# Performance work log

Hardware: AMD Instinct MI355X
Metric: run time of the kernel (lower is better)

## Reference

```python
import jax, jax.numpy as jnp
import numpy as np

N = 50000
E = 800000
EPS = 1e-5
GAT_SLOPE = 0.2   # PyG GATConv internal LeakyReLU slope
ACT_SLOPE = 0.01  # decoder's LeakyReLU(alpha)


def setup_inputs() -> dict:
    key = jax.random.key(0)
    ks = jax.random.split(key, 10)
    d = {
        "embeddings": jax.random.normal(ks[0], (N, 64), jnp.float32),
        "edge_index": jax.random.randint(ks[1], (2, E), 0, N, jnp.int64),
        "W1": jax.random.normal(ks[2], (64, 128), jnp.float32) * 0.1,
        "a_src1": jax.random.normal(ks[3], (128,), jnp.float32) * 0.1,
        "a_dst1": jax.random.normal(ks[4], (128,), jnp.float32) * 0.1,
        "b1": jnp.zeros((128,), jnp.float32),
        "gamma1": jnp.ones((128,), jnp.float32),
        "beta1": jnp.zeros((128,), jnp.float32),
        "W2": jax.random.normal(ks[5], (128, 256), jnp.float32) * 0.1,
        "a_src2": jax.random.normal(ks[6], (256,), jnp.float32) * 0.1,
        "a_dst2": jax.random.normal(ks[7], (256,), jnp.float32) * 0.1,
        "b2": jnp.zeros((256,), jnp.float32),
        "gamma2": jnp.ones((256,), jnp.float32),
        "beta2": jnp.zeros((256,), jnp.float32),
        "Wf": jax.random.normal(ks[8], (256, 256), jnp.float32) * 0.1,
        "bf": jnp.zeros((256,), jnp.float32),
    }
    return d


def gat_conv(x, src, dst, W, a_s, a_d, b):
    # PyG GATConv, heads=1, concat=False, add_self_loops=True (loops appended in caller)
    h = x @ W                                    # [N, out]
    e = h @ a_s                                  # alpha_src per node
    f = h @ a_d                                  # alpha_dst per node
    logits = jax.nn.leaky_relu(e[src] + f[dst], GAT_SLOPE)   # [E']
    # scatter-softmax over destination neighborhoods
    m = jax.ops.segment_max(logits, dst, num_segments=N)
    ex = jnp.exp(logits - m[dst])
    denom = jax.ops.segment_sum(ex, dst, num_segments=N)
    alpha = ex / denom[dst]                      # [E']
    out = jax.ops.segment_sum(h[src] * alpha[:, None], dst, num_segments=N)
    return out + b


def batch_norm(x, gamma, beta):
    mu = jnp.mean(x, axis=0)
    var = jnp.mean((x - mu) ** 2, axis=0)        # biased, as torch BN uses
    return (x - mu) * jax.lax.rsqrt(var + EPS) * gamma + beta


def reference(embeddings, edge_index, W1, a_src1, a_dst1, b1, gamma1, beta1,
              W2, a_src2, a_dst2, b2, gamma2, beta2, Wf, bf):
    loops = jnp.arange(N, dtype=edge_index.dtype)
    src = jnp.concatenate([edge_index[0], loops])
    dst = jnp.concatenate([edge_index[1], loops])
    x = embeddings
    for (W, a_s, a_d, b, g, be) in [
        (W1, a_src1, a_dst1, b1, gamma1, beta1),
        (W2, a_src2, a_dst2, b2, gamma2, beta2),
    ]:
        x = gat_conv(x, src, dst, W, a_s, a_d, b)
        x = batch_norm(x, g, be)
        x = jax.nn.leaky_relu(x, ACT_SLOPE)
        # dropout: identity (eval mode)
    return x @ Wf + bf
```

## Files before the change

kernel.cpp:

```cpp
#include <hip/hip_runtime.h>
#include <hip/hip_fp16.h>
#include <math.h>

#define N_NODES 50000
#define N_EDGES 800000
#define N_TOT   850000
#define EPS_BN  1e-5f
#define GAT_SLOPE 0.2f
#define ACT_SLOPE 0.01f
#define NBUCK   ((N_NODES + 255) / 256)
#define BCAP    5120
#define K1_CH   4096
#define K1_NB   ((N_TOT + K1_CH - 1) / K1_CH)
#define GB64    ((N_NODES + 63) / 64)

typedef _Float16 half8_t __attribute__((ext_vector_type(8)));
typedef _Float16 half4_t __attribute__((ext_vector_type(4)));
typedef _Float16 half2_t __attribute__((ext_vector_type(2)));
typedef float    f32x4   __attribute__((ext_vector_type(4)));

__device__ __forceinline__ float wred_max(float x) {
#pragma unroll
    for (int m = 32; m; m >>= 1) x = fmaxf(x, __shfl_xor(x, m, 64));
    return x;
}
__device__ __forceinline__ float wred_sum(float x) {
#pragma unroll
    for (int m = 32; m; m >>= 1) x += __shfl_xor(x, m, 64);
    return x;
}
__device__ __forceinline__ int wred_sum_i(int x) {
#pragma unroll
    for (int m = 32; m; m >>= 1) x += __shfl_xor(x, m, 64);
    return x;
}

__device__ __forceinline__ void wf_perm(const float* __restrict__ W,
                                        _Float16* __restrict__ wt,
                                        int K, int C, int i) {
    int j   = i & 7;
    int l   = (i >> 3) & 63;
    int rest = i >> 9;
    int tt  = rest & 3;
    int ksf = rest >> 2;
    int KS  = K >> 5;
    int cb  = ksf / KS, ks = ksf - cb * KS;
    int k   = ks * 32 + (l >> 4) * 8 + j;
    int c   = cb * 64 + tt * 16 + (l & 15);
    wt[i] = (_Float16)W[k * C + c];
}

__global__ void init_misc(const float* __restrict__ W1, const float* __restrict__ W2,
                          const float* __restrict__ Wf, _Float16* __restrict__ wt1,
                          _Float16* __restrict__ wt2, _Float16* __restrict__ wtf,
                          int* __restrict__ bcnt,
                          const float* __restrict__ as1, const float* __restrict__ ad1,
                          const float* __restrict__ as2, const float* __restrict__ ad2,
                          float* __restrict__ va1, float* __restrict__ vb1,
                          float* __restrict__ va2, float* __restrict__ vb2) {
    int i = blockIdx.x * 256 + threadIdx.x;
    if (i < NBUCK) bcnt[i] = 0;
    if (i < 8192) {
        wf_perm(W1, wt1, 64, 128, i);
    } else if (i < 8192 + 32768) {
        wf_perm(W2, wt2, 128, 256, i - 8192);
    } else if (i < 8192 + 32768 + 65536) {
        wf_perm(Wf, wtf, 256, 256, i - 40960);
    } else if (i < 106496 + 384) {
        int j = i - 106496;
        if (j < 64) {
            float s = 0.f;
            for (int c = 0; c < 128; ++c) s += W1[j * 128 + c] * as1[c];
            va1[j] = s;
        } else if (j < 128) {
            int k = j - 64; float s = 0.f;
            for (int c = 0; c < 128; ++c) s += W1[k * 128 + c] * ad1[c];
            vb1[k] = s;
        } else if (j < 256) {
            int k = j - 128; float s = 0.f;
            for (int c = 0; c < 256; ++c) s += W2[k * 256 + c] * as2[c];
            va2[k] = s;
        } else {
            int k = j - 256; float s = 0.f;
            for (int c = 0; c < 256; ++c) s += W2[k * 256 + c] * ad2[c];
            vb2[k] = s;
        }
    }
}

__global__ __launch_bounds__(256) void
emb_dots(const float* __restrict__ emb, const float* __restrict__ va,
         const float* __restrict__ vb, _Float16* __restrict__ embh,
         float* __restrict__ e_n, float* __restrict__ f_n) {
    int r = blockIdx.x * 4 + (threadIdx.x >> 6);
    if (r >= N_NODES) return;
    int l = threadIdx.x & 63;
    float v = emb[(size_t)r * 64 + l];
    embh[(size_t)r * 64 + l] = (_Float16)v;
    float pe = wred_sum(v * va[l]);
    float pf = wred_sum(v * vb[l]);
    if (l == 0) { e_n[r] = pe; f_n[r] = pf; }
}

__global__ __launch_bounds__(256) void
ef_dots(const _Float16* __restrict__ x, const float* __restrict__ sc,
        const float* __restrict__ sh, const float* __restrict__ va,
        const float* __restrict__ vb, _Float16* __restrict__ z,
        float* __restrict__ e_n, float* __restrict__ f_n) {
    int r = blockIdx.x * 4 + (threadIdx.x >> 6);
    if (r >= N_NODES) return;
    int l = threadIdx.x & 63;
    int c = 2 * l;
    half2_t hv = *(const half2_t*)&x[(size_t)r * 128 + c];
    float x0 = (float)hv[0] * sc[c] + sh[c];
    float x1 = (float)hv[1] * sc[c + 1] + sh[c + 1];
    x0 = x0 > 0.f ? x0 : ACT_SLOPE * x0;
    x1 = x1 > 0.f ? x1 : ACT_SLOPE * x1;
    half2_t zo = { (_Float16)x0, (_Float16)x1 };
    *(half2_t*)&z[(size_t)r * 128 + c] = zo;
    float pe = wred_sum(x0 * va[c] + x1 * va[c + 1]);
    float pf = wred_sum(x0 * vb[c] + x1 * vb[c + 1]);
    if (l == 0) { e_n[r] = pe; f_n[r] = pf; }
}

template<int K, int C, int CB, typename InT, typename OutT, bool STATS>
__global__ __launch_bounds__(256) void
gemm_mfma(const InT* __restrict__ x, const _Float16* __restrict__ wt,
          const float* __restrict__ bias, OutT* __restrict__ out, int n,
          const float* __restrict__ scale, const float* __restrict__ shift,
          float2* __restrict__ pbn) {
    constexpr int NW_C = CB / 64;
    constexpr int RT   = NW_C;
    constexpr int NCB  = C / CB;
    constexpr int KS   = K / 32;
    constexpr int LK   = K + 8;
    constexpr int LCB  = CB + 4;
    constexpr size_t SMB = ((size_t)64 * LK * 2 > (size_t)64 * LCB * 4)
                             ? (size_t)64 * LK * 2 : (size_t)64 * LCB * 4;
    __shared__ alignas(16) char smem[SMB];
    _Float16* xs  = (_Float16*)smem;
    float*   cbuf = (float*)smem;
    __shared__ float cs_sh[STATS ? CB : 1];
    __shared__ float cq_sh[STATS ? CB : 1];

    const int rb = blockIdx.x / NCB;
    const int cblk = blockIdx.x - rb * NCB;
    const int row0 = rb * 64;
    const int colB = cblk * CB;
    const int t = threadIdx.x;

    if (STATS) {
        for (int c = t; c < CB; c += 256) { cs_sh[c] = 0.f; cq_sh[c] = 0.f; }
    }

    if constexpr (__is_same(InT, _Float16)) {
        for (int i = t * 8; i < 64 * K; i += 256 * 8) {
            int r = i / K, c = i - (i / K) * K;
            half8_t v = {};
            if (row0 + r < n) v = *(const half8_t*)&x[(size_t)(row0 + r) * K + c];
            if (scale) {
#pragma unroll
                for (int j = 0; j < 8; ++j) {
                    float f = (float)v[j] * scale[c + j] + shift[c + j];
                    v[j] = (_Float16)(f > 0.f ? f : ACT_SLOPE * f);
                }
            }
            *(half8_t*)&xs[r * LK + c] = v;
        }
    } else {
        for (int i = t * 4; i < 64 * K; i += 256 * 4) {
            int r = i / K, c = i - (i / K) * K;
            float4 v = make_float4(0.f, 0.f, 0.f, 0.f);
            if (row0 + r < n) v = *(const float4*)&x[(size_t)(row0 + r) * K + c];
            if (scale) {
                v.x = v.x * scale[c] + shift[c];         v.x = v.x > 0.f ? v.x : ACT_SLOPE * v.x;
                v.y = v.y * scale[c + 1] + shift[c + 1]; v.y = v.y > 0.f ? v.y : ACT_SLOPE * v.y;
                v.z = v.z * scale[c + 2] + shift[c + 2]; v.z = v.z > 0.f ? v.z : ACT_SLOPE * v.z;
                v.w = v.w * scale[c + 3] + shift[c + 3]; v.w = v.w > 0.f ? v.w : ACT_SLOPE * v.w;
            }
            half4_t h4 = { (_Float16)v.x, (_Float16)v.y, (_Float16)v.z, (_Float16)v.w };
            *(half4_t*)&xs[r * LK + c] = h4;
        }
    }
    __syncthreads();

    const int w = t >> 6, l = t & 63;
    const int l16 = l & 15, quad = l >> 4;
    const int lc0 = (w % NW_C) * 64;
    const int gc0 = colB + lc0;
    const int mbase = (w / NW_C) * (16 * NW_C);
    const _Float16* wtw = wt + (size_t)(gc0 >> 6) * KS * 4 * 512 + l * 8;

    f32x4 acc[RT][4] = {};
    half8_t bA[4], bB[4];
    auto loadB = [&](int k0, half8_t* bf) {
        const _Float16* p = wtw + (size_t)(k0 >> 5) * 4 * 512;
#pragma unroll
        for (int tt = 0; tt < 4; ++tt)
            bf[tt] = *(const half8_t*)&p[tt * 512];
    };
    auto doMM = [&](int k0, half8_t* bf) {
        half8_t a[RT];
#pragma unroll
        for (int rt = 0; rt < RT; ++rt)
            a[rt] = *(const half8_t*)&xs[(mbase + rt * 16 + l16) * LK + k0 + quad * 8];
#pragma unroll
        for (int rt = 0; rt < RT; ++rt)
#pragma unroll
            for (int tt = 0; tt < 4; ++tt)
                acc[rt][tt] = __builtin_amdgcn_mfma_f32_16x16x32_f16(a[rt], bf[tt],
                                                                     acc[rt][tt], 0, 0, 0);
    };
    loadB(0, bA);
#pragma unroll
    for (int k0 = 0; k0 < K; k0 += 64) {
        loadB(k0 + 32, bB);
        doMM(k0, bA);
        if (k0 + 64 < K) loadB(k0 + 64, bA);
        doMM(k0 + 32, bB);
    }

    __syncthreads();
#pragma unroll
    for (int rt = 0; rt < RT; ++rt) {
#pragma unroll
        for (int tt = 0; tt < 4; ++tt) {
            int lcol = lc0 + tt * 16 + l16;
            float bb = bias ? bias[colB + lcol] : 0.f;
            float s = 0.f, q = 0.f;
#pragma unroll
            for (int i = 0; i < 4; ++i) {
                int lrow = mbase + rt * 16 + quad * 4 + i;
                float v = acc[rt][tt][i] + bb;
                cbuf[lrow * LCB + lcol] = v;
                if (STATS && row0 + lrow < n) { s += v; q += v * v; }
            }
            if constexpr (STATS) {
                s += __shfl_xor(s, 16, 64); s += __shfl_xor(s, 32, 64);
                q += __shfl_xor(q, 16, 64); q += __shfl_xor(q, 32, 64);
                if (quad == 0) {
                    atomicAdd(&cs_sh[lcol], s);
                    atomicAdd(&cq_sh[lcol], q);
                }
            }
        }
    }
    __syncthreads();
    if constexpr (STATS) {
        for (int c = t; c < CB; c += 256)
            pbn[(size_t)rb * C + colB + c] = make_float2(cs_sh[c], cq_sh[c]);
    }
    for (int i = t * 4; i < 64 * CB; i += 256 * 4) {
        int r = i / CB, c = i - (i / CB) * CB;
        if (row0 + r < n) {
            float4 v4 = *(const float4*)&cbuf[r * LCB + c];
            if constexpr (__is_same(OutT, float)) {
                *(float4*)&out[(size_t)(row0 + r) * C + colB + c] = v4;
            } else {
                half4_t h4 = { (_Float16)v4.x, (_Float16)v4.y,
                               (_Float16)v4.z, (_Float16)v4.w };
                *(half4_t*)&out[(size_t)(row0 + r) * C + colB + c] = h4;
            }
        }
    }
}

__global__ __launch_bounds__(256) void
bucket_append(const int* __restrict__ ei, int* __restrict__ bcnt,
              unsigned* __restrict__ bedge) {
    __shared__ int lcnt[NBUCK], lrank[NBUCK], gbase[NBUCK];
    const int t = threadIdx.x;
    const int base = blockIdx.x * K1_CH;
    const int nE = min(K1_CH, N_TOT - base);
    for (int i = t; i < NBUCK; i += 256) { lcnt[i] = 0; lrank[i] = 0; }
    __syncthreads();
    for (int i = t; i < nE; i += 256) {
        int e = base + i;
        int d = (e < N_EDGES) ? ei[N_EDGES + e] : (e - N_EDGES);
        atomicAdd(&lcnt[d >> 8], 1);
    }
    __syncthreads();
    if (t < NBUCK && lcnt[t] > 0) gbase[t] = atomicAdd(&bcnt[t], lcnt[t]);
    __syncthreads();
    for (int i = t; i < nE; i += 256) {
        int e = base + i;
        int s, d;
        if (e < N_EDGES) { s = ei[e]; d = ei[N_EDGES + e]; }
        else { s = e - N_EDGES; d = s; }
        int bk = d >> 8;
        int gp = gbase[bk] + atomicAdd(&lrank[bk], 1);
        if (gp < BCAP)
            bedge[(size_t)bk * BCAP + gp] = ((unsigned)d << 16) | (unsigned)s;
    }
}

__global__ __launch_bounds__(256) void
bucket_csr(const int* __restrict__ bcnt, const unsigned* __restrict__ bedge,
           int* __restrict__ ptr, int* __restrict__ srcs) {
    __shared__ int lcnt[256], lptr[256], lrank[256];
    __shared__ int wsum[4];
    __shared__ int sbase;
    const int b = blockIdx.x, t = threadIdx.x;
    lcnt[t] = 0; lrank[t] = 0;
    if (t < 64) {
        int s = 0;
        for (int j = t; j < b; j += 64) s += bcnt[j];
        s = wred_sum_i(s);
        if (t == 0) sbase = s;
    }
    __syncthreads();
    const int cnt = min(bcnt[b], BCAP);
    const int base0 = sbase;
    const unsigned* eb = bedge + (size_t)b * BCAP;
    for (int i = t; i < cnt; i += 256) atomicAdd(&lcnt[(eb[i] >> 16) & 255], 1);
    __syncthreads();
    int lane = t & 63, w = t >> 6;
    int v = lcnt[t];
    int x = v;
#pragma unroll
    for (int off = 1; off < 64; off <<= 1) {
        int y = __shfl_up(x, off, 64);
        if (lane >= off) x += y;
    }
    if (lane == 63) wsum[w] = x;
    __syncthreads();
    if (t == 0) {
        int s = 0;
#pragma unroll
        for (int i = 0; i < 4; ++i) { int tmp = wsum[i]; wsum[i] = s; s += tmp; }
    }
    __syncthreads();
    lptr[t] = x - v + wsum[w];
    __syncthreads();
    int d = b * 256 + t;
    if (d < N_NODES) ptr[d] = base0 + lptr[t];
    if (b == NBUCK - 1 && t == 0) ptr[N_NODES] = base0 + cnt;
    for (int i = t; i < cnt; i += 256) {
        unsigned v2 = eb[i];
        int dl = (v2 >> 16) & 255;
        int pos = base0 + lptr[dl] + atomicAdd(&lrank[dl], 1);
        srcs[pos] = (int)(v2 & 0xFFFFu);
    }
}

template<int C>
__global__ __launch_bounds__(256) void
attn_aggregate(const _Float16* __restrict__ h, const int* __restrict__ srcs,
               const int* __restrict__ ptr, const float* __restrict__ e_n,
               const float* __restrict__ f_n, _Float16* __restrict__ out) {
    constexpr int RL = C / 8;
    constexpr int G  = 64 / RL;
    int d = blockIdx.x * 4 + (threadIdx.x >> 6);
    if (d >= N_NODES) return;
    int l  = threadIdx.x & 63;
    int b0 = ptr[d], b1 = ptr[d + 1];
    int deg = b1 - b0;
    float fd = f_n[d];
    const int g  = l / RL;
    const int cl = l % RL;
    float acc[8] = {0.f, 0.f, 0.f, 0.f, 0.f, 0.f, 0.f, 0.f};

    if (deg <= 64) {
        int sj = 0; float lg = -1e30f;
        if (l < deg) {
            sj = srcs[b0 + l];
            float v = e_n[sj] + fd;
            lg = v > 0.f ? v : GAT_SLOPE * v;
        }
        float m  = wred_max(lg);
        float e0 = (l < deg) ? __expf(lg - m) : 0.f;
        float ex = e0 / wred_sum(e0);

        int jj = 0;
        for (; jj + 4 * G <= deg; jj += 4 * G) {
            float wk[4]; int sk[4];
#pragma unroll
            for (int k = 0; k < 4; ++k) {
                int j = jj + k * G + g;
                wk[k] = __shfl(ex, j, 64);
                sk[k] = __shfl(sj, j, 64);
            }
            half8_t v[4];
#pragma unroll
            for (int k = 0; k < 4; ++k)
                v[k] = *(const half8_t*)&h[(size_t)sk[k] * C + cl * 8];
#pragma unroll
            for (int k = 0; k < 4; ++k)
#pragma unroll
                for (int i = 0; i < 8; ++i)
                    acc[i] += wk[k] * (float)v[k][i];
        }
        for (; jj + 2 * G <= deg; jj += 2 * G) {
            float w1 = __shfl(ex, jj + g, 64);
            int   s1 = __shfl(sj, jj + g, 64);
            float w2 = __shfl(ex, jj + G + g, 64);
            int   s2 = __shfl(sj, jj + G + g, 64);
            half8_t v1 = *(const half8_t*)&h[(size_t)s1 * C + cl * 8];
            half8_t v2 = *(const half8_t*)&h[(size_t)s2 * C + cl * 8];
#pragma unroll
            for (int i = 0; i < 8; ++i)
                acc[i] += w1 * (float)v1[i] + w2 * (float)v2[i];
        }
        for (; jj < deg; jj += G) {
            int j = jj + g;
            float wk = __shfl(ex, j, 64);
            int   sk = __shfl(sj, j, 64);
            if (j < deg) {
                half8_t v = *(const half8_t*)&h[(size_t)sk * C + cl * 8];
#pragma unroll
                for (int i = 0; i < 8; ++i) acc[i] += wk * (float)v[i];
            }
        }
    } else {
        float m_l = -1e30f, den_l = 0.f;
        for (int j = b0 + l; j < b1; j += 64) {
            float lg = e_n[srcs[j]] + fd;
            lg = lg > 0.f ? lg : GAT_SLOPE * lg;
            float nm = fmaxf(m_l, lg);
            den_l = den_l * __expf(m_l - nm) + __expf(lg - nm);
            m_l = nm;
        }
        float m = wred_max(m_l);
        float inv = 1.f / wred_sum(den_l * __expf(m_l - m));
        for (int c0 = b0; c0 < b1; c0 += 64) {
            int jl = c0 + l;
            int sj = 0; float ex = 0.f;
            if (jl < b1) {
                sj = srcs[jl];
                float lg = e_n[sj] + fd;
                lg = lg > 0.f ? lg : GAT_SLOPE * lg;
                ex = __expf(lg - m) * inv;
            }
            int nE = min(64, b1 - c0);
            for (int jj = 0; jj < nE; jj += 2 * G) {
                int j1 = jj + g, j2 = jj + G + g;
                float w1 = __shfl(ex, j1, 64);
                int   s1 = __shfl(sj, j1, 64);
                float w2 = __shfl(ex, j2, 64);
                int   s2 = __shfl(sj, j2, 64);
                half8_t v1 = *(const half8_t*)&h[(size_t)s1 * C + cl * 8];
                half8_t v2 = *(const half8_t*)&h[(size_t)s2 * C + cl * 8];
#pragma unroll
                for (int i = 0; i < 8; ++i)
                    acc[i] += w1 * (float)v1[i] + w2 * (float)v2[i];
            }
        }
    }
#pragma unroll
    for (int mm = RL; mm < 64; mm <<= 1)
#pragma unroll
        for (int i = 0; i < 8; ++i) acc[i] += __shfl_xor(acc[i], mm, 64);
    if (g == 0) {
        int c = cl * 8;
        half8_t o;
#pragma unroll
        for (int i = 0; i < 8; ++i) o[i] = (_Float16)acc[i];
        *(half8_t*)&out[(size_t)d * C + c] = o;
    }
}

template<int C, int PB>
__global__ __launch_bounds__(256) void
bn_coef(const float2* __restrict__ partial, const float* __restrict__ gamma,
        const float* __restrict__ beta, float* __restrict__ scale,
        float* __restrict__ shift) {
    int w = threadIdx.x >> 6, l = threadIdx.x & 63;
    int c = blockIdx.x * 4 + w;
    float s = 0.f, q = 0.f;
    for (int b = l; b < PB; b += 64) {
        float2 p = partial[(size_t)b * C + c];
        s += p.x; q += p.y;
    }
    s = wred_sum(s); q = wred_sum(q);
    if (l == 0) {
        float mu  = s / N_NODES;
        float var = q / N_NODES - mu * mu;
        float sc = gamma[c] * rsqrtf(var + EPS_BN);
        scale[c] = sc;
        shift[c] = beta[c] - mu * sc;
    }
}

extern "C" void kernel_launch(void* const* d_in, const int* in_sizes, int n_in,
                              void* d_out, int out_size, void* d_ws, size_t ws_size,
                              hipStream_t stream) {
    const float* emb  = (const float*)d_in[0];
    const int*   ei   = (const int*)  d_in[1];
    const float* W1   = (const float*)d_in[2];
    const float* as1  = (const float*)d_in[3];
    const float* ad1  = (const float*)d_in[4];
    const float* b1   = (const float*)d_in[5];
    const float* g1   = (const float*)d_in[6];
    const float* be1  = (const float*)d_in[7];
    const float* W2   = (const float*)d_in[8];
    const float* as2  = (const float*)d_in[9];
    const float* ad2  = (const float*)d_in[10];
    const float* b2   = (const float*)d_in[11];
    const float* g2   = (const float*)d_in[12];
    const float* be2  = (const float*)d_in[13];
    const float* Wf   = (const float*)d_in[14];
    const float* bf   = (const float*)d_in[15];
    float* out = (float*)d_out;

    char* w = (char*)d_ws;
    auto alloc = [&](size_t bytes) {
        char* p = w;
        w += (bytes + 255) & ~(size_t)255;
        return (void*)p;
    };
    _Float16* embh = (_Float16*)alloc((size_t)N_NODES * 64 * 2);
    _Float16* agg1 = (_Float16*)alloc((size_t)N_NODES * 64 * 2);
    _Float16* out1 = (_Float16*)alloc((size_t)N_NODES * 128 * 2);
    _Float16* agg2 = (_Float16*)alloc((size_t)N_NODES * 128 * 2);
    _Float16* out2 = (_Float16*)alloc((size_t)N_NODES * 256 * 2);
    _Float16* z1h  = embh;
    unsigned* bedge = (unsigned*)out2;
    float*  e_n  = (float*) alloc((size_t)N_NODES * 4);
    float*  f_n  = (float*) alloc((size_t)N_NODES * 4);
    int*    srcs = (int*)   alloc((size_t)N_TOT * 4);
    int*    bcnt = (int*)   alloc((size_t)NBUCK * 4);
    int*    ptr  = (int*)   alloc((size_t)(N_NODES + 1) * 4);
    float2* pbn  = (float2*)alloc((size_t)GB64 * 256 * 8);
    float*  sc1  = (float*) alloc(128 * 4);
    float*  sh1  = (float*) alloc(128 * 4);
    float*  sc2  = (float*) alloc(256 * 4);
    float*  sh2  = (float*) alloc(256 * 4);
    float*  va1  = (float*) alloc(64 * 4);
    float*  vb1  = (float*) alloc(64 * 4);
    float*  va2  = (float*) alloc(128 * 4);
    float*  vb2  = (float*) alloc(128 * 4);
    _Float16* wt1 = (_Float16*)alloc((size_t)64 * 128 * 2);
    _Float16* wt2 = (_Float16*)alloc((size_t)128 * 256 * 2);
    _Float16* wtf = (_Float16*)alloc((size_t)256 * 256 * 2);

    const int RW4 = (N_NODES + 3) / 4;

    init_misc<<<(106496 + 384 + 255) / 256, 256, 0, stream>>>(
        W1, W2, Wf, wt1, wt2, wtf, bcnt, as1, ad1, as2, ad2, va1, vb1, va2, vb2);

    emb_dots<<<RW4, 256, 0, stream>>>(emb, va1, vb1, embh, e_n, f_n);

    bucket_append<<<K1_NB, 256, 0, stream>>>(ei, bcnt, bedge);
    bucket_csr<<<NBUCK, 256, 0, stream>>>(bcnt, bedge, ptr, srcs);

    attn_aggregate<64><<<RW4, 256, 0, stream>>>(embh, srcs, ptr, e_n, f_n, agg1);
    gemm_mfma<64, 128, 128, _Float16, _Float16, true><<<GB64, 256, 0, stream>>>(
        agg1, wt1, b1, out1, N_NODES, nullptr, nullptr, pbn);
    bn_coef<128, GB64><<<128 / 4, 256, 0, stream>>>(pbn, g1, be1, sc1, sh1);

    ef_dots<<<RW4, 256, 0, stream>>>(out1, sc1, sh1, va2, vb2, z1h, e_n, f_n);
    attn_aggregate<128><<<RW4, 256, 0, stream>>>(z1h, srcs, ptr, e_n, f_n, agg2);
    gemm_mfma<128, 256, 128, _Float16, _Float16, true><<<GB64 * 2, 256, 0, stream>>>(
        agg2, wt2, b2, out2, N_NODES, nullptr, nullptr, pbn);
    bn_coef<256, GB64><<<256 / 4, 256, 0, stream>>>(pbn, g2, be2, sc2, sh2);

    gemm_mfma<256, 256, 128, _Float16, float, false><<<GB64 * 2, 256, 0, stream>>>(
        out2, wtf, bf, out, N_NODES, sc2, sh2, nullptr);
}
```

Measured before the change: 291.0 us.

## Fuse bucket append with embedding dots and fold BN coefficients into GEMM tail

Merges the edge bucketing kernel and the embedding dot-product kernel into one launch that dispatches on block index. Edge values are cached in registers instead of re-read in a second pass. The separate bn_coef kernels are removed: each stats GEMM publishes its partial sums atomically, and the last block to finish (found through a global done counter) reduces them and writes scale and shift. This cuts launch count and serialization between kernels, but the final reduction now runs in a single block, which adds a serial tail.

```diff
diff --git a/kernel.cpp b/kernel.cpp
--- a/kernel.cpp
+++ b/kernel.cpp
@@ -33,6 +33,14 @@
 #pragma unroll
     for (int m = 32; m; m >>= 1) x += __shfl_xor(x, m, 64);
     return x;
+}
+
+__device__ __forceinline__ unsigned long long sq_pack(float s, float q) {
+    return ((unsigned long long)__float_as_uint(q) << 32) | __float_as_uint(s);
+}
+__device__ __forceinline__ void sq_unpack(unsigned long long u, float& s, float& q) {
+    s = __uint_as_float((unsigned)u);
+    q = __uint_as_float((unsigned)(u >> 32));
 }
 
 __device__ __forceinline__ void wf_perm(const float* __restrict__ W,
@@ -53,13 +61,14 @@
 __global__ void init_misc(const float* __restrict__ W1, const float* __restrict__ W2,
                           const float* __restrict__ Wf, _Float16* __restrict__ wt1,
                           _Float16* __restrict__ wt2, _Float16* __restrict__ wtf,
-                          int* __restrict__ bcnt,
+                          int* __restrict__ bcnt, int* __restrict__ gcnt,
                           const float* __restrict__ as1, const float* __restrict__ ad1,
                           const float* __restrict__ as2, const float* __restrict__ ad2,
                           float* __restrict__ va1, float* __restrict__ vb1,
                           float* __restrict__ va2, float* __restrict__ vb2) {
     int i = blockIdx.x * 256 + threadIdx.x;
     if (i < NBUCK) bcnt[i] = 0;
+    if (i < 2) gcnt[i] = 0;
     if (i < 8192) {
         wf_perm(W1, wt1, 64, 128, i);
     } else if (i < 8192 + 32768) {
@@ -89,17 +98,103 @@
 }
 
 __global__ __launch_bounds__(256) void
-emb_dots(const float* __restrict__ emb, const float* __restrict__ va,
-         const float* __restrict__ vb, _Float16* __restrict__ embh,
-         float* __restrict__ e_n, float* __restrict__ f_n) {
-    int r = blockIdx.x * 4 + (threadIdx.x >> 6);
-    if (r >= N_NODES) return;
-    int l = threadIdx.x & 63;
-    float v = emb[(size_t)r * 64 + l];
-    embh[(size_t)r * 64 + l] = (_Float16)v;
+append_emb(const int* __restrict__ ei, int* __restrict__ bcnt,
+           unsigned* __restrict__ bedge,
+           const float* __restrict__ emb, const float* __restrict__ va,
+           const float* __restrict__ vb, _Float16* __restrict__ embh,
+           float* __restrict__ e_n, float* __restrict__ f_n) {
+    const int t = threadIdx.x;
+    if ((int)blockIdx.x < K1_NB) {
+        __shared__ int lcnt[NBUCK], lrank[NBUCK], gbase[NBUCK];
+        const int base = blockIdx.x * K1_CH;
+        const int nE = min(K1_CH, N_TOT - base);
+        for (int i = t; i < NBUCK; i += 256) { lcnt[i] = 0; lrank[i] = 0; }
+        __syncthreads();
+        unsigned r[16];
+#pragma unroll
+        for (int j = 0; j < 16; ++j) {
+            int i = t + j * 256;
+            if (i < nE) {
+                int e = base + i;
+                int s, d;
+                if (e < N_EDGES) { s = ei[e]; d = ei[N_EDGES + e]; }
+                else { s = e - N_EDGES; d = s; }
+                r[j] = ((unsigned)d << 16) | (unsigned)s;
+                atomicAdd(&lcnt[d >> 8], 1);
+            }
+        }
+        __syncthreads();
+        if (t < NBUCK && lcnt[t] > 0) gbase[t] = atomicAdd(&bcnt[t], lcnt[t]);
+        __syncthreads();
+#pragma unroll
+        for (int j = 0; j < 16; ++j) {
+            int i = t + j * 256;
+            if (i < nE) {
+                unsigned v = r[j];
+                int bk = v >> 24;
+                int gp = gbase[bk] + atomicAdd(&lrank[bk], 1);
+                if (gp < BCAP) bedge[(size_t)bk * BCAP + gp] = v;
+            }
+        }
+        return;
+    }
+    int rr = ((int)blockIdx.x - K1_NB) * 4 + (t >> 6);
+    if (rr >= N_NODES) return;
+    int l = t & 63;
+    float v = emb[(size_t)rr * 64 + l];
+    embh[(size_t)rr * 64 + l] = (_Float16)v;
     float pe = wred_sum(v * va[l]);
     float pf = wred_sum(v * vb[l]);
-    if (l == 0) { e_n[r] = pe; f_n[r] = pf; }
+    if (l == 0) { e_n[rr] = pe; f_n[rr] = pf; }
+}
+
+__global__ __launch_bounds__(256) void
+bucket_csr(const int* __restrict__ bcnt, const unsigned* __restrict__ bedge,
+           int* __restrict__ ptr, int* __restrict__ srcs) {
+    __shared__ int lcnt[256], lptr[256], lrank[256];
+    __shared__ int wsum[4];
+    __shared__ int sbase;
+    const int b = blockIdx.x, t = threadIdx.x;
+    lcnt[t] = 0; lrank[t] = 0;
+    if (t < 64) {
+        int s = 0;
+        for (int j = t; j < b; j += 64) s += bcnt[j];
+        s = wred_sum_i(s);
+        if (t == 0) sbase = s;
+    }
+    __syncthreads();
+    const int cnt = min(bcnt[b], BCAP);
+    const int base0 = sbase;
+    const unsigned* eb = bedge + (size_t)b * BCAP;
+    for (int i = t; i < cnt; i += 256) atomicAdd(&lcnt[(eb[i] >> 16) & 255], 1);
+    __syncthreads();
+    int lane = t & 63, w = t >> 6;
+    int v = lcnt[t];
+    int x = v;
+#pragma unroll
+    for (int off = 1; off < 64; off <<= 1) {
+        int y = __shfl_up(x, off, 64);
+        if (lane >= off) x += y;
+    }
+    if (lane == 63) wsum[w] = x;
+    __syncthreads();
+    if (t == 0) {
+        int s = 0;
+#pragma unroll
+        for (int i = 0; i < 4; ++i) { int tmp = wsum[i]; wsum[i] = s; s += tmp; }
+    }
+    __syncthreads();
+    lptr[t] = x - v + wsum[w];
+    __syncthreads();
+    int d = b * 256 + t;
+    if (d < N_NODES) ptr[d] = base0 + lptr[t];
+    if (b == NBUCK - 1 && t == 0) ptr[N_NODES] = base0 + cnt;
+    for (int i = t; i < cnt; i += 256) {
+        unsigned v2 = eb[i];
+        int dl = (v2 >> 16) & 255;
+        int pos = base0 + lptr[dl] + atomicAdd(&lrank[dl], 1);
+        srcs[pos] = (int)(v2 & 0xFFFFu);
+    }
 }
 
 __global__ __launch_bounds__(256) void
@@ -128,7 +223,10 @@
 gemm_mfma(const InT* __restrict__ x, const _Float16* __restrict__ wt,
           const float* __restrict__ bias, OutT* __restrict__ out, int n,
           const float* __restrict__ scale, const float* __restrict__ shift,
-          float2* __restrict__ pbn) {
+          float2* __restrict__ pbn,
+          const float* __restrict__ gamma, const float* __restrict__ beta,
+          float* __restrict__ o_scale, float* __restrict__ o_shift,
+          int* __restrict__ done) {
     constexpr int NW_C = CB / 64;
     constexpr int RT   = NW_C;
     constexpr int NCB  = C / CB;
@@ -248,7 +346,10 @@
     __syncthreads();
     if constexpr (STATS) {
         for (int c = t; c < CB; c += 256)
-            pbn[(size_t)rb * C + colB + c] = make_float2(cs_sh[c], cq_sh[c]);
+            __hip_atomic_store(
+                (unsigned long long*)&pbn[(size_t)rb * C + colB + c],
+                sq_pack(cs_sh[c], cq_sh[c]),
+                __ATOMIC_RELAXED, __HIP_MEMORY_SCOPE_AGENT);
     }
     for (int i = t * 4; i < 64 * CB; i += 256 * 4) {
         int r = i / CB, c = i - (i / CB) * CB;
@@ -263,83 +364,35 @@
             }
         }
     }
-}
-
-__global__ __launch_bounds__(256) void
-bucket_append(const int* __restrict__ ei, int* __restrict__ bcnt,
-              unsigned* __restrict__ bedge) {
-    __shared__ int lcnt[NBUCK], lrank[NBUCK], gbase[NBUCK];
-    const int t = threadIdx.x;
-    const int base = blockIdx.x * K1_CH;
-    const int nE = min(K1_CH, N_TOT - base);
-    for (int i = t; i < NBUCK; i += 256) { lcnt[i] = 0; lrank[i] = 0; }
-    __syncthreads();
-    for (int i = t; i < nE; i += 256) {
-        int e = base + i;
-        int d = (e < N_EDGES) ? ei[N_EDGES + e] : (e - N_EDGES);
-        atomicAdd(&lcnt[d >> 8], 1);
-    }
-    __syncthreads();
-    if (t < NBUCK && lcnt[t] > 0) gbase[t] = atomicAdd(&bcnt[t], lcnt[t]);
-    __syncthreads();
-    for (int i = t; i < nE; i += 256) {
-        int e = base + i;
-        int s, d;
-        if (e < N_EDGES) { s = ei[e]; d = ei[N_EDGES + e]; }
-        else { s = e - N_EDGES; d = s; }
-        int bk = d >> 8;
-        int gp = gbase[bk] + atomicAdd(&lrank[bk], 1);
-        if (gp < BCAP)
-            bedge[(size_t)bk * BCAP + gp] = ((unsigned)d << 16) | (unsigned)s;
-    }
-}
-
-__global__ __launch_bounds__(256) void
-bucket_csr(const int* __restrict__ bcnt, const unsigned* __restrict__ bedge,
-           int* __restrict__ ptr, int* __restrict__ srcs) {
-    __shared__ int lcnt[256], lptr[256], lrank[256];
-    __shared__ int wsum[4];
-    __shared__ int sbase;
-    const int b = blockIdx.x, t = threadIdx.x;
-    lcnt[t] = 0; lrank[t] = 0;
-    if (t < 64) {
-        int s = 0;
-        for (int j = t; j < b; j += 64) s += bcnt[j];
-        s = wred_sum_i(s);
-        if (t == 0) sbase = s;
-    }
-    __syncthreads();
-    const int cnt = min(bcnt[b], BCAP);
-    const int base0 = sbase;
-    const unsigned* eb = bedge + (size_t)b * BCAP;
-    for (int i = t; i < cnt; i += 256) atomicAdd(&lcnt[(eb[i] >> 16) & 255], 1);
-    __syncthreads();
-    int lane = t & 63, w = t >> 6;
-    int v = lcnt[t];
-    int x = v;
-#pragma unroll
-    for (int off = 1; off < 64; off <<= 1) {
-        int y = __shfl_up(x, off, 64);
-        if (lane >= off) x += y;
-    }
-    if (lane == 63) wsum[w] = x;
-    __syncthreads();
-    if (t == 0) {
-        int s = 0;
-#pragma unroll
-        for (int i = 0; i < 4; ++i) { int tmp = wsum[i]; wsum[i] = s; s += tmp; }
-    }
-    __syncthreads();
-    lptr[t] = x - v + wsum[w];
-    __syncthreads();
-    int d = b * 256 + t;
-    if (d < N_NODES) ptr[d] = base0 + lptr[t];
-    if (b == NBUCK - 1 && t == 0) ptr[N_NODES] = base0 + cnt;
-    for (int i = t; i < cnt; i += 256) {
-        unsigned v2 = eb[i];
-        int dl = (v2 >> 16) & 255;
-        int pos = base0 + lptr[dl] + atomicAdd(&lrank[dl], 1);
-        srcs[pos] = (int)(v2 & 0xFFFFu);
+
+    if constexpr (STATS) {
+        __shared__ bool isLast;
+        __syncthreads();
+        if (t == 0) {
+            int old = __hip_atomic_fetch_add(done, 1, __ATOMIC_ACQ_REL,
+                                             __HIP_MEMORY_SCOPE_AGENT);
+            isLast = (old == (int)gridDim.x - 1);
+        }
+        __syncthreads();
+        if (isLast) {
+            const int PB = (int)gridDim.x / NCB;
+            for (int c = t; c < C; c += 256) {
+                float s = 0.f, q = 0.f;
+                for (int b = 0; b < PB; ++b) {
+                    float ps, pq;
+                    sq_unpack(__hip_atomic_load(
+                                  (const unsigned long long*)&pbn[(size_t)b * C + c],
+                                  __ATOMIC_RELAXED, __HIP_MEMORY_SCOPE_AGENT),
+                              ps, pq);
+                    s += ps; q += pq;
+                }
+                float mu  = s / N_NODES;
+                float var = q / N_NODES - mu * mu;
+                float scv = gamma[c] * rsqrtf(var + EPS_BN);
+                o_scale[c] = scv;
+                o_shift[c] = beta[c] - mu * scv;
+            }
+        }
     }
 }
 
@@ -456,28 +509,6 @@
 #pragma unroll
         for (int i = 0; i < 8; ++i) o[i] = (_Float16)acc[i];
         *(half8_t*)&out[(size_t)d * C + c] = o;
-    }
-}
-
-template<int C, int PB>
-__global__ __launch_bounds__(256) void
-bn_coef(const float2* __restrict__ partial, const float* __restrict__ gamma,
-        const float* __restrict__ beta, float* __restrict__ scale,
-        float* __restrict__ shift) {
-    int w = threadIdx.x >> 6, l = threadIdx.x & 63;
-    int c = blockIdx.x * 4 + w;
-    float s = 0.f, q = 0.f;
-    for (int b = l; b < PB; b += 64) {
-        float2 p = partial[(size_t)b * C + c];
-        s += p.x; q += p.y;
-    }
-    s = wred_sum(s); q = wred_sum(q);
-    if (l == 0) {
-        float mu  = s / N_NODES;
-        float var = q / N_NODES - mu * mu;
-        float sc = gamma[c] * rsqrtf(var + EPS_BN);
-        scale[c] = sc;
-        shift[c] = beta[c] - mu * sc;
     }
 }
 
@@ -519,6 +550,7 @@
     float*  f_n  = (float*) alloc((size_t)N_NODES * 4);
     int*    srcs = (int*)   alloc((size_t)N_TOT * 4);
     int*    bcnt = (int*)   alloc((size_t)NBUCK * 4);
+    int*    gcnt = (int*)   alloc(2 * 4);
     int*    ptr  = (int*)   alloc((size_t)(N_NODES + 1) * 4);
     float2* pbn  = (float2*)alloc((size_t)GB64 * 256 * 8);
     float*  sc1  = (float*) alloc(128 * 4);
@@ -536,24 +568,28 @@
     const int RW4 = (N_NODES + 3) / 4;
 
     init_misc<<<(106496 + 384 + 255) / 256, 256, 0, stream>>>(
-        W1, W2, Wf, wt1, wt2, wtf, bcnt, as1, ad1, as2, ad2, va1, vb1, va2, vb2);
-
-    emb_dots<<<RW4, 256, 0, stream>>>(emb, va1, vb1, embh, e_n, f_n);
-
-    bucket_append<<<K1_NB, 256, 0, stream>>>(ei, bcnt, bedge);
+        W1, W2, Wf, wt1, wt2, wtf, bcnt, gcnt,
+        as1, ad1, as2, ad2, va1, vb1, va2, vb2);
+
+    append_emb<<<K1_NB + RW4, 256, 0, stream>>>(
+        ei, bcnt, bedge, emb, va1, vb1, embh, e_n, f_n);
+
     bucket_csr<<<NBUCK, 256, 0, stream>>>(bcnt, bedge, ptr, srcs);
 
     attn_aggregate<64><<<RW4, 256, 0, stream>>>(embh, srcs, ptr, e_n, f_n, agg1);
+
     gemm_mfma<64, 128, 128, _Float16, _Float16, true><<<GB64, 256, 0, stream>>>(
-        agg1, wt1, b1, out1, N_NODES, nullptr, nullptr, pbn);
-    bn_coef<128, GB64><<<128 / 4, 256, 0, stream>>>(pbn, g1, be1, sc1, sh1);
+        agg1, wt1, b1, out1, N_NODES, nullptr, nullptr, pbn, g1, be1, sc1, sh1, gcnt);
 
     ef_dots<<<RW4, 256, 0, stream>>>(out1, sc1, sh1, va2, vb2, z1h, e_n, f_n);
+
     attn_aggregate<128><<<RW4, 256, 0, stream>>>(z1h, srcs, ptr, e_n, f_n, agg2);
+
     gemm_mfma<128, 256, 128, _Float16, _Float16, true><<<GB64 * 2, 256, 0, stream>>>(
-        agg2, wt2, b2, out2, N_NODES, nullptr, nullptr, pbn);
-    bn_coef<256, GB64><<<256 / 4, 256, 0, stream>>>(pbn, g2, be2, sc2, sh2);
+        agg2, wt2, b2, out2, N_NODES, nullptr, nullptr, pbn, g2, be2, sc2, sh2,
+        gcnt + 1);
 
     gemm_mfma<256, 256, 128, _Float16, float, false><<<GB64 * 2, 256, 0, stream>>>(
-        out2, wtf, bf, out, N_NODES, sc2, sh2, nullptr);
-}
+        out2, wtf, bf, out, N_NODES, sc2, sh2, nullptr,
+        nullptr, nullptr, nullptr, nullptr, nullptr);
+}
```

Result: slower. 729.1 us (+150.5%).
